# Performance work log

Measured on AMD Instinct MI355X. Metric: run time of the kernel, lower is better.

The kernel has to match this reference:

```python
import jax, jax.numpy as jnp
import numpy as np

N, E = 50000, 600000
DIMS = [128, 256, 256, 256, 256, 64]  # in, h1..h4, out


def setup_inputs() -> dict:
    key = jax.random.key(0)
    ks = jax.random.split(key, 12)
    inp = {
        "x": jax.random.normal(ks[0], (N, DIMS[0]), dtype=jnp.float32),
        "edge_index": jax.random.randint(ks[1], (2, E), 0, N, dtype=jnp.int64 if jax.config.jax_enable_x64 else jnp.int32),
    }
    for i in range(5):
        fi, fo = DIMS[i], DIMS[i + 1]
        s = 1.0 / np.sqrt(fi)  # glorot-ish uniform, matching GCNConv default scale
        inp[f"W{i+1}"] = jax.random.uniform(ks[2 + 2 * i], (fi, fo), jnp.float32, -s, s)
        inp[f"b{i+1}"] = jnp.zeros((fo,), jnp.float32)
    return inp


def _gcn_norm(edge_index, n):
    # Add self-loops and compute symmetric normalization D^-1/2 (A+I) D^-1/2.
    loop = jnp.arange(n, dtype=edge_index.dtype)
    src = jnp.concatenate([edge_index[0], loop])  # [E+N]
    dst = jnp.concatenate([edge_index[1], loop])
    deg = jax.ops.segment_sum(jnp.ones_like(dst, dtype=jnp.float32), dst, num_segments=n)
    dinv = jnp.where(deg > 0, jax.lax.rsqrt(deg), 0.0)
    norm = dinv[src] * dinv[dst]  # [E+N]
    return src, dst, norm


def _gcn_layer(x, src, dst, norm, W, b, n):
    h = x @ W                       # [N, Fo] linear transform first (fewer msg bytes)
    msg = h[src] * norm[:, None]    # gather + edge-weight scale
    out = jax.ops.segment_sum(msg, dst, num_segments=n)  # scatter-add aggregate
    return out + b


def reference(x, edge_index, W1, b1, W2, b2, W3, b3, W4, b4, W5, b5):
    n = x.shape[0]
    src, dst, norm = _gcn_norm(edge_index, n)
    params = [(W1, b1), (W2, b2), (W3, b3), (W4, b4), (W5, b5)]
    h = x
    for i, (W, b) in enumerate(params):
        h = _gcn_layer(h, src, dst, norm, W, b, n)
        if i < 4:
            h = jax.nn.relu(h)  # dropout is identity in eval mode
    return h
```

## Files before the change

### kernel.cpp

```cpp
#include <hip/hip_runtime.h>
#include <stdint.h>


typedef _Float16 v8h __attribute__((ext_vector_type(8)));
typedef _Float16 v4h __attribute__((ext_vector_type(4)));
typedef _Float16 v2h __attribute__((ext_vector_type(2)));
typedef float v4f __attribute__((ext_vector_type(4)));
typedef float v16f __attribute__((ext_vector_type(16)));

__global__ void count_edges(const int* __restrict__ dst, int E, int* __restrict__ counts) {
    int i = blockIdx.x * blockDim.x + threadIdx.x;
    if (i < E) atomicAdd(&counts[dst[i]], 1);
}

__global__ void block_sums(const int* __restrict__ counts, int n, int* __restrict__ partial) {
    __shared__ int red[256];
    int t = threadIdx.x;
    int i = blockIdx.x * 256 + t;
    red[t] = (i < n) ? counts[i] : 0;
    __syncthreads();
    #pragma unroll
    for (int off = 128; off > 0; off >>= 1) {
        if (t < off) red[t] += red[t + off];
        __syncthreads();
    }
    if (t == 0) partial[blockIdx.x] = red[0];
}

__global__ void scan_partials(int* __restrict__ partial, int nb, int* __restrict__ row_ptr, int n) {
    __shared__ int s[256];
    int t = threadIdx.x;
    int v = (t < nb) ? partial[t] : 0;
    s[t] = v;
    __syncthreads();
    #pragma unroll
    for (int off = 1; off < 256; off <<= 1) {
        int u = (t >= off) ? s[t - off] : 0;
        __syncthreads();
        s[t] += u;
        __syncthreads();
    }
    if (t < nb) partial[t] = s[t] - v;
    if (t == 0) row_ptr[n] = s[255];
}

__global__ void scan_final(const int* __restrict__ counts, int n, const int* __restrict__ partial,
                           int* __restrict__ row_ptr, float* __restrict__ dinv,
                           int* __restrict__ fill) {
    __shared__ int s[256];
    int t = threadIdx.x;
    int i = blockIdx.x * 256 + t;
    int c = (i < n) ? counts[i] : 0;
    s[t] = c;
    __syncthreads();
    #pragma unroll
    for (int off = 1; off < 256; off <<= 1) {
        int u = (t >= off) ? s[t - off] : 0;
        __syncthreads();
        s[t] += u;
        __syncthreads();
    }
    if (i < n) {
        row_ptr[i] = partial[blockIdx.x] + s[t] - c;
        dinv[i] = rsqrtf((float)(c + 1));
        fill[i] = 0;
    }
}

__global__ void build_csr(const int* __restrict__ src, const int* __restrict__ dst, int E,
                          const int* __restrict__ row_ptr, int* __restrict__ fill,
                          int2* __restrict__ esw, const float* __restrict__ dinv) {
    int i = blockIdx.x * blockDim.x + threadIdx.x;
    if (i < E) {
        int d = dst[i];
        int s = src[i];
        int pos = row_ptr[d] + atomicAdd(&fill[d], 1);
        esw[pos] = make_int2(s, __float_as_int(dinv[s]));
    }
}

struct SplitArgs {
    const float* W[5];
    _Float16* Wh[5];
    _Float16* Wl[5];
    int lgFI[5];
    int FO[5];
    int off[6];
};

__global__ void split_all(SplitArgs a) {
    int i = blockIdx.x * 256 + threadIdx.x;
    #pragma unroll
    for (int l = 0; l < 5; ++l) {
        if (i >= a.off[l] && i < a.off[l + 1]) {
            int j = i - a.off[l];
            int FI = 1 << a.lgFI[l];
            int c = j >> a.lgFI[l];
            int k = j & (FI - 1);
            float v = a.W[l][(size_t)k * a.FO[l] + c];
            _Float16 h = (_Float16)v;
            a.Wh[l][j] = h;
            a.Wl[l][j] = (_Float16)(v - (float)h);
        }
    }
}

__global__ __launch_bounds__(256) void agg_packed(
    const _Float16* __restrict__ inP, const int* __restrict__ row_ptr,
    const int2* __restrict__ esw, const float* __restrict__ dinv,
    _Float16* __restrict__ outH, _Float16* __restrict__ outL, int n) {
    int wid = (blockIdx.x * blockDim.x + threadIdx.x) >> 6;
    if (wid >= n) return;
    const int lane = threadIdx.x & 63;
    int e = __builtin_amdgcn_readfirstlane(row_ptr[wid]);
    const int end = __builtin_amdgcn_readfirstlane(row_ptr[wid + 1]);
    const float dd = dinv[wid];
    const _Float16* rb = inP + (size_t)lane * 8;
    float a0, a1, a2, a3;
    {
        v8h p = *(const v8h*)(rb + (size_t)wid * 512);
        a0 = dd * ((float)p[0] + (float)p[1]);
        a1 = dd * ((float)p[2] + (float)p[3]);
        a2 = dd * ((float)p[4] + (float)p[5]);
        a3 = dd * ((float)p[6] + (float)p[7]);
    }
#define GTH(q) (*(const v8h*)(rb + (size_t)(q).x * 512))
#define ACC(b, w)                                  \
    a0 += (w) * ((float)(b)[0] + (float)(b)[1]);   \
    a1 += (w) * ((float)(b)[2] + (float)(b)[3]);   \
    a2 += (w) * ((float)(b)[4] + (float)(b)[5]);   \
    a3 += (w) * ((float)(b)[6] + (float)(b)[7]);
    for (; e + 8 <= end; e += 8) {
        int2 q0 = esw[e + 0], q1 = esw[e + 1], q2 = esw[e + 2], q3 = esw[e + 3];
        int2 q4 = esw[e + 4], q5 = esw[e + 5], q6 = esw[e + 6], q7 = esw[e + 7];
        v8h b0 = GTH(q0), b1 = GTH(q1), b2 = GTH(q2), b3 = GTH(q3);
        v8h b4 = GTH(q4), b5 = GTH(q5), b6 = GTH(q6), b7 = GTH(q7);
        ACC(b0, __int_as_float(q0.y)) ACC(b1, __int_as_float(q1.y))
        ACC(b2, __int_as_float(q2.y)) ACC(b3, __int_as_float(q3.y))
        ACC(b4, __int_as_float(q4.y)) ACC(b5, __int_as_float(q5.y))
        ACC(b6, __int_as_float(q6.y)) ACC(b7, __int_as_float(q7.y))
    }
    if (e + 4 <= end) {
        int2 q0 = esw[e + 0], q1 = esw[e + 1], q2 = esw[e + 2], q3 = esw[e + 3];
        v8h b0 = GTH(q0), b1 = GTH(q1), b2 = GTH(q2), b3 = GTH(q3);
        ACC(b0, __int_as_float(q0.y)) ACC(b1, __int_as_float(q1.y))
        ACC(b2, __int_as_float(q2.y)) ACC(b3, __int_as_float(q3.y))
        e += 4;
    }
    if (e < end) {
        const int em = end - 1;
        int e1 = (e + 1 < end) ? e + 1 : em;
        int e2 = (e + 2 < end) ? e + 2 : em;
        int2 q0 = esw[e], q1 = esw[e1], q2 = esw[e2], q3 = esw[em];
        float w0 = __int_as_float(q0.y);
        float w1 = (e + 1 < end) ? __int_as_float(q1.y) : 0.f;
        float w2 = (e + 2 < end) ? __int_as_float(q2.y) : 0.f;
        float w3 = (e + 3 < end) ? __int_as_float(q3.y) : 0.f;
        v8h b0 = GTH(q0), b1 = GTH(q1), b2 = GTH(q2), b3 = GTH(q3);
        ACC(b0, w0) ACC(b1, w1) ACC(b2, w2) ACC(b3, w3)
    }
#undef GTH
#undef ACC
    size_t o = (size_t)wid * 256 + lane * 4;
    float s0 = dd * a0, s1 = dd * a1, s2 = dd * a2, s3 = dd * a3;
    _Float16 h0 = (_Float16)s0, h1 = (_Float16)s1, h2 = (_Float16)s2, h3 = (_Float16)s3;
    *(v4h*)&outH[o] = (v4h){h0, h1, h2, h3};
    *(v4h*)&outL[o] = (v4h){(_Float16)(s0 - (float)h0), (_Float16)(s1 - (float)h1),
                            (_Float16)(s2 - (float)h2), (_Float16)(s3 - (float)h3)};
}

__global__ __launch_bounds__(256) void agg_f32_128(
    const float* __restrict__ in, const int* __restrict__ row_ptr,
    const int2* __restrict__ esw, const float* __restrict__ dinv,
    _Float16* __restrict__ outH, _Float16* __restrict__ outL, int n) {
    int wid = (blockIdx.x * blockDim.x + threadIdx.x) >> 6;
    if (wid >= n) return;
    const int lane = threadIdx.x & 63;
    int e = __builtin_amdgcn_readfirstlane(row_ptr[wid]);
    const int end = __builtin_amdgcn_readfirstlane(row_ptr[wid + 1]);
    const float dd = dinv[wid];
    const float* rb = in + (size_t)lane * 2;
    float a0, a1;
    {
        float2 p = *(const float2*)(rb + (size_t)wid * 128);
        a0 = dd * p.x;
        a1 = dd * p.y;
    }
#define GTH(q) (*(const float2*)(rb + (size_t)(q).x * 128))
#define ACC(b, w) a0 += (w) * (b).x; a1 += (w) * (b).y;
    for (; e + 8 <= end; e += 8) {
        int2 q0 = esw[e + 0], q1 = esw[e + 1], q2 = esw[e + 2], q3 = esw[e + 3];
        int2 q4 = esw[e + 4], q5 = esw[e + 5], q6 = esw[e + 6], q7 = esw[e + 7];
        float2 b0 = GTH(q0), b1 = GTH(q1), b2 = GTH(q2), b3 = GTH(q3);
        float2 b4 = GTH(q4), b5 = GTH(q5), b6 = GTH(q6), b7 = GTH(q7);
        ACC(b0, __int_as_float(q0.y)) ACC(b1, __int_as_float(q1.y))
        ACC(b2, __int_as_float(q2.y)) ACC(b3, __int_as_float(q3.y))
        ACC(b4, __int_as_float(q4.y)) ACC(b5, __int_as_float(q5.y))
        ACC(b6, __int_as_float(q6.y)) ACC(b7, __int_as_float(q7.y))
    }
    if (e + 4 <= end) {
        int2 q0 = esw[e + 0], q1 = esw[e + 1], q2 = esw[e + 2], q3 = esw[e + 3];
        float2 b0 = GTH(q0), b1 = GTH(q1), b2 = GTH(q2), b3 = GTH(q3);
        ACC(b0, __int_as_float(q0.y)) ACC(b1, __int_as_float(q1.y))
        ACC(b2, __int_as_float(q2.y)) ACC(b3, __int_as_float(q3.y))
        e += 4;
    }
    if (e < end) {
        const int em = end - 1;
        int e1 = (e + 1 < end) ? e + 1 : em;
        int e2 = (e + 2 < end) ? e + 2 : em;
        int2 q0 = esw[e], q1 = esw[e1], q2 = esw[e2], q3 = esw[em];
        float w0 = __int_as_float(q0.y);
        float w1 = (e + 1 < end) ? __int_as_float(q1.y) : 0.f;
        float w2 = (e + 2 < end) ? __int_as_float(q2.y) : 0.f;
        float w3 = (e + 3 < end) ? __int_as_float(q3.y) : 0.f;
        float2 b0 = GTH(q0), b1 = GTH(q1), b2 = GTH(q2), b3 = GTH(q3);
        ACC(b0, w0) ACC(b1, w1) ACC(b2, w2) ACC(b3, w3)
    }
#undef GTH
#undef ACC
    size_t o = (size_t)wid * 128 + lane * 2;
    float s0 = dd * a0, s1 = dd * a1;
    _Float16 h0 = (_Float16)s0, h1 = (_Float16)s1;
    *(v2h*)&outH[o] = (v2h){h0, h1};
    *(v2h*)&outL[o] = (v2h){(_Float16)(s0 - (float)h0), (_Float16)(s1 - (float)h1)};
}

__global__ __launch_bounds__(256) void agg_f32_64(
    const float* __restrict__ in, const int* __restrict__ row_ptr,
    const int2* __restrict__ esw, const float* __restrict__ dinv,
    const float* __restrict__ bias, float* __restrict__ outF, int n) {
    int wid = (blockIdx.x * blockDim.x + threadIdx.x) >> 6;
    if (wid >= n) return;
    const int lane = threadIdx.x & 63;
    int e = __builtin_amdgcn_readfirstlane(row_ptr[wid]);
    const int end = __builtin_amdgcn_readfirstlane(row_ptr[wid + 1]);
    const float dd = dinv[wid];
    const float* rb = in + lane;
    float a0 = dd * rb[(size_t)wid * 64];
#define GTH(q) (rb[(size_t)(q).x * 64])
    for (; e + 8 <= end; e += 8) {
        int2 q0 = esw[e + 0], q1 = esw[e + 1], q2 = esw[e + 2], q3 = esw[e + 3];
        int2 q4 = esw[e + 4], q5 = esw[e + 5], q6 = esw[e + 6], q7 = esw[e + 7];
        float b0 = GTH(q0), b1 = GTH(q1), b2 = GTH(q2), b3 = GTH(q3);
        float b4 = GTH(q4), b5 = GTH(q5), b6 = GTH(q6), b7 = GTH(q7);
        a0 += __int_as_float(q0.y) * b0 + __int_as_float(q1.y) * b1;
        a0 += __int_as_float(q2.y) * b2 + __int_as_float(q3.y) * b3;
        a0 += __int_as_float(q4.y) * b4 + __int_as_float(q5.y) * b5;
        a0 += __int_as_float(q6.y) * b6 + __int_as_float(q7.y) * b7;
    }
    if (e + 4 <= end) {
        int2 q0 = esw[e + 0], q1 = esw[e + 1], q2 = esw[e + 2], q3 = esw[e + 3];
        float b0 = GTH(q0), b1 = GTH(q1), b2 = GTH(q2), b3 = GTH(q3);
        a0 += __int_as_float(q0.y) * b0 + __int_as_float(q1.y) * b1;
        a0 += __int_as_float(q2.y) * b2 + __int_as_float(q3.y) * b3;
        e += 4;
    }
    if (e < end) {
        const int em = end - 1;
        int e1 = (e + 1 < end) ? e + 1 : em;
        int e2 = (e + 2 < end) ? e + 2 : em;
        int2 q0 = esw[e], q1 = esw[e1], q2 = esw[e2], q3 = esw[em];
        float w0 = __int_as_float(q0.y);
        float w1 = (e + 1 < end) ? __int_as_float(q1.y) : 0.f;
        float w2 = (e + 2 < end) ? __int_as_float(q2.y) : 0.f;
        float w3 = (e + 3 < end) ? __int_as_float(q3.y) : 0.f;
        float b0 = GTH(q0), b1 = GTH(q1), b2 = GTH(q2), b3 = GTH(q3);
        a0 += w0 * b0 + w1 * b1 + w2 * b2 + w3 * b3;
    }
#undef GTH
    outF[(size_t)wid * 64 + lane] = dd * a0 + bias[lane];
}

__device__ __forceinline__ void gl_lds16(const _Float16* g, _Float16* l) {
    __builtin_amdgcn_global_load_lds(
        (const __attribute__((address_space(1))) uint32_t*)g,
        (__attribute__((address_space(3))) uint32_t*)l, 16, 0, 0);
}

template <int FI, int OUTMODE>
__global__ __launch_bounds__(256) void gemm_wide(
    const _Float16* __restrict__ Ah, const _Float16* __restrict__ Al,
    const _Float16* __restrict__ Wth, const _Float16* __restrict__ Wtl,
    const float* __restrict__ bias,
    uint32_t* __restrict__ Opk, _Float16* __restrict__ Oh, _Float16* __restrict__ Ol,
    int n) {
    constexpr int BK = 32;
    constexpr int NSTEP = FI / BK;
    __shared__ _Float16 lds[20480];
    const int m0 = blockIdx.x * 64;
    const int t = threadIdx.x;
    const int w = t >> 6;
    const int lane = t & 63;

    const int arow = w * 16 + (lane & 15);
    const int akc = (lane >> 4) * 8;
    const _Float16* sAh = Ah + (size_t)(m0 + arow) * FI + akc;
    const _Float16* sAl = Al + (size_t)(m0 + arow) * FI + akc;
    _Float16* dAh = &lds[w * 512];
    _Float16* dAl = &lds[2048 + w * 512];
    size_t boff[4];
    #pragma unroll
    for (int q = 0; q < 4; ++q)
        boff[q] = (size_t)((w * 4 + q) * 16 + (lane & 15)) * FI + akc;

    v16f acc[2][2];
    #pragma unroll
    for (int i = 0; i < 2; ++i)
        #pragma unroll
        for (int j = 0; j < 2; ++j) acc[i][j] = (v16f)(0.f);

    const int rsel = (lane >> 4) & 1;
    const int kq = lane >> 5;
    const int l8 = (lane & 15) * 8;

    for (int s = 0; s < NSTEP; ++s) {
        const int ko = s * BK;
        gl_lds16(sAh + ko, dAh);
        gl_lds16(sAl + ko, dAl);
        #pragma unroll
        for (int q = 0; q < 4; ++q) {
            gl_lds16(Wth + boff[q] + ko, &lds[4096 + (w * 4 + q) * 512]);
            gl_lds16(Wtl + boff[q] + ko, &lds[12288 + (w * 4 + q) * 512]);
        }
        __syncthreads();
        v8h ah[2][2], al[2][2], bh[2][2], bl[2][2];
        #pragma unroll
        for (int i = 0; i < 2; ++i)
            #pragma unroll
            for (int ks = 0; ks < 2; ++ks) {
                const int aoff = (i * 2 + rsel) * 512 + (ks * 2 + kq) * 128 + l8;
                ah[i][ks] = *(const v8h*)&lds[aoff];
                al[i][ks] = *(const v8h*)&lds[2048 + aoff];
            }
        #pragma unroll
        for (int j = 0; j < 2; ++j)
            #pragma unroll
            for (int ks = 0; ks < 2; ++ks) {
                const int bo = 4096 + (w * 4 + j * 2 + rsel) * 512 + (ks * 2 + kq) * 128 + l8;
                bh[j][ks] = *(const v8h*)&lds[bo];
                bl[j][ks] = *(const v8h*)&lds[bo + 8192];
            }
        #pragma unroll
        for (int i = 0; i < 2; ++i)
            #pragma unroll
            for (int j = 0; j < 2; ++j)
                #pragma unroll
                for (int ks = 0; ks < 2; ++ks) {
                    acc[i][j] = __builtin_amdgcn_mfma_f32_32x32x16_f16(ah[i][ks], bh[j][ks], acc[i][j], 0, 0, 0);
                    acc[i][j] = __builtin_amdgcn_mfma_f32_32x32x16_f16(ah[i][ks], bl[j][ks], acc[i][j], 0, 0, 0);
                    acc[i][j] = __builtin_amdgcn_mfma_f32_32x32x16_f16(al[i][ks], bh[j][ks], acc[i][j], 0, 0, 0);
                }
        __syncthreads();
    }

    const int col = lane & 31;
    const int rb4 = (lane >> 5) * 4;
    #pragma unroll
    for (int j = 0; j < 2; ++j) {
        const int gcol = w * 64 + j * 32 + col;
        const float bv = bias[gcol];
        #pragma unroll
        for (int i = 0; i < 2; ++i) {
            #pragma unroll
            for (int reg = 0; reg < 16; ++reg) {
                const int row = (reg & 3) + 8 * (reg >> 2) + rb4;
                const int grow = m0 + i * 32 + row;
                if (grow < n) {
                    float v = fmaxf(acc[i][j][reg] + bv, 0.f);
                    _Float16 h = (_Float16)v;
                    _Float16 l = (_Float16)(v - (float)h);
                    if (OUTMODE == 0) {
                        uint32_t u = (uint32_t)__builtin_bit_cast(uint16_t, h) |
                                     ((uint32_t)__builtin_bit_cast(uint16_t, l) << 16);
                        Opk[(size_t)grow * 256 + gcol] = u;
                    } else {
                        Oh[(size_t)grow * 256 + gcol] = h;
                        Ol[(size_t)grow * 256 + gcol] = l;
                    }
                }
            }
        }
    }
}

__global__ __launch_bounds__(256) void gemm_narrow(
    const _Float16* __restrict__ Ah, const _Float16* __restrict__ Al,
    const _Float16* __restrict__ Wth, const _Float16* __restrict__ Wtl,
    float* __restrict__ Of, int n) {
    constexpr int FI = 256, FO = 64;
    __shared__ _Float16 lds[12288];
    const int m0 = blockIdx.x * 128;
    const int t = threadIdx.x;
    const int w = t >> 6;
    const int lane = t & 63;

    const int G0 = w * 128 + lane;
    const int G1 = G0 + 64;
    const int arow0 = (G0 >> 6) * 16 + (G0 & 15), akc0 = ((G0 >> 4) & 3) * 8;
    const int arow1 = (G1 >> 6) * 16 + (G1 & 15), akc1 = ((G1 >> 4) & 3) * 8;
    const _Float16* sAh0 = Ah + (size_t)(m0 + arow0) * FI + akc0;
    const _Float16* sAh1 = Ah + (size_t)(m0 + arow1) * FI + akc1;
    const _Float16* sAl0 = Al + (size_t)(m0 + arow0) * FI + akc0;
    const _Float16* sAl1 = Al + (size_t)(m0 + arow1) * FI + akc1;
    const int bcol = w * 16 + (lane & 15), bkc = (lane >> 4) * 8;
    const _Float16* sBh = Wth + (size_t)bcol * FI + bkc;
    const _Float16* sBl = Wtl + (size_t)bcol * FI + bkc;

    _Float16* dAh0 = &lds[w * 1024];
    _Float16* dAh1 = &lds[w * 1024 + 512];
    _Float16* dAl0 = &lds[4096 + w * 1024];
    _Float16* dAl1 = &lds[4096 + w * 1024 + 512];
    _Float16* dBh = &lds[8192 + w * 512];
    _Float16* dBl = &lds[10240 + w * 512];

    const int wm = w >> 1, wn = w & 1;
    v4f acc[4][2];
    #pragma unroll
    for (int i = 0; i < 4; ++i)
        #pragma unroll
        for (int j = 0; j < 2; ++j) acc[i][j] = (v4f){0.f, 0.f, 0.f, 0.f};

    for (int s = 0; s < 8; ++s) {
        const int ko = s * 32;
        gl_lds16(sAh0 + ko, dAh0);
        gl_lds16(sAh1 + ko, dAh1);
        gl_lds16(sAl0 + ko, dAl0);
        gl_lds16(sAl1 + ko, dAl1);
        gl_lds16(sBh + ko, dBh);
        gl_lds16(sBl + ko, dBl);
        __syncthreads();
        v8h ah[4], al[4], bh[2], bl[2];
        #pragma unroll
        for (int i = 0; i < 4; ++i) {
            ah[i] = *(const v8h*)&lds[(wm * 4 + i) * 512 + lane * 8];
            al[i] = *(const v8h*)&lds[4096 + (wm * 4 + i) * 512 + lane * 8];
        }
        #pragma unroll
        for (int j = 0; j < 2; ++j) {
            bh[j] = *(const v8h*)&lds[8192 + (wn * 2 + j) * 512 + lane * 8];
            bl[j] = *(const v8h*)&lds[10240 + (wn * 2 + j) * 512 + lane * 8];
        }
        #pragma unroll
        for (int i = 0; i < 4; ++i)
            #pragma unroll
            for (int j = 0; j < 2; ++j) {
                acc[i][j] = __builtin_amdgcn_mfma_f32_16x16x32_f16(ah[i], bh[j], acc[i][j], 0, 0, 0);
                acc[i][j] = __builtin_amdgcn_mfma_f32_16x16x32_f16(ah[i], bl[j], acc[i][j], 0, 0, 0);
                acc[i][j] = __builtin_amdgcn_mfma_f32_16x16x32_f16(al[i], bh[j], acc[i][j], 0, 0, 0);
            }
        __syncthreads();
    }

    const int rl = (lane >> 4) * 4;
    const int cl = lane & 15;
    #pragma unroll
    for (int j = 0; j < 2; ++j) {
        const int gcol = wn * 32 + j * 16 + cl;
        #pragma unroll
        for (int i = 0; i < 4; ++i) {
            const int grow = m0 + wm * 64 + i * 16 + rl;
            #pragma unroll
            for (int r = 0; r < 4; ++r)
                if (grow + r < n) Of[(size_t)(grow + r) * FO + gcol] = acc[i][j][r];
        }
    }
}

extern "C" void kernel_launch(void* const* d_in, const int* in_sizes, int n_in,
                              void* d_out, int out_size, void* d_ws, size_t ws_size,
                              hipStream_t stream) {
    const float* x = (const float*)d_in[0];
    const int* ei = (const int*)d_in[1];
    const int E = in_sizes[1] / 2;
    const int n = in_sizes[0] / 128;
    const int* esrc = ei;
    const int* edst = ei + E;
    const float* b[5] = {(const float*)d_in[3], (const float*)d_in[5], (const float*)d_in[7],
                         (const float*)d_in[9], (const float*)d_in[11]};
    float* out = (float*)d_out;
    const int NPAD = ((n + 127) / 128) * 128;

    char* ws = (char*)d_ws;
    auto carve = [&](size_t bytes) {
        char* p = ws;
        ws += (bytes + 255) & ~(size_t)255;
        return p;
    };
    int* counts = (int*)carve((size_t)n * 4);
    int* row_ptr = (int*)carve((size_t)(n + 1) * 4);
    int* fill = (int*)carve((size_t)n * 4);
    float* dinv = (float*)carve((size_t)n * 4);
    int* partial = (int*)carve(1024);
    int2* esw = (int2*)carve((size_t)E * 8);
    const int FIs[5] = {128, 256, 256, 256, 256};
    const int FOs[5] = {256, 256, 256, 256, 64};
    _Float16 *Wh[5], *Wl[5];
    for (int l = 0; l < 5; ++l) {
        Wh[l] = (_Float16*)carve((size_t)FIs[l] * FOs[l] * 2);
        Wl[l] = (_Float16*)carve((size_t)FIs[l] * FOs[l] * 2);
    }
    _Float16* Ah = (_Float16*)carve((size_t)NPAD * 256 * 2);
    _Float16* Al = (_Float16*)carve((size_t)NPAD * 256 * 2);
    uint32_t* Ppk = (uint32_t*)carve((size_t)NPAD * 256 * 4);
    _Float16* Bh2 = (_Float16*)Ppk;
    _Float16* Bl2 = (_Float16*)Ppk + (size_t)NPAD * 256;
    float* scratch = (float*)Ah;

    hipMemsetAsync(counts, 0, (size_t)n * 4, stream);
    count_edges<<<(E + 255) / 256, 256, 0, stream>>>(edst, E, counts);
    const int nsb = (n + 255) / 256;
    block_sums<<<nsb, 256, 0, stream>>>(counts, n, partial);
    scan_partials<<<1, 256, 0, stream>>>(partial, nsb, row_ptr, n);
    scan_final<<<nsb, 256, 0, stream>>>(counts, n, partial, row_ptr, dinv, fill);
    build_csr<<<(E + 255) / 256, 256, 0, stream>>>(esrc, edst, E, row_ptr, fill, esw, dinv);

    SplitArgs sa;
    int off = 0;
    for (int l = 0; l < 5; ++l) {
        sa.W[l] = (const float*)d_in[2 + 2 * l];
        sa.Wh[l] = Wh[l];
        sa.Wl[l] = Wl[l];
        sa.lgFI[l] = (FIs[l] == 128) ? 7 : 8;
        sa.FO[l] = FOs[l];
        sa.off[l] = off;
        off += FIs[l] * FOs[l];
    }
    sa.off[5] = off;
    split_all<<<(off + 255) / 256, 256, 0, stream>>>(sa);

    const int aggBlocks = (n + 3) / 4;
    const int gw = NPAD / 64;
    const int gn = NPAD / 128;

    agg_f32_128<<<aggBlocks, 256, 0, stream>>>(x, row_ptr, esw, dinv, Ah, Al, n);
    gemm_wide<128, 0><<<gw, 256, 0, stream>>>(Ah, Al, Wh[0], Wl[0], b[0], Ppk, nullptr, nullptr, n);
    for (int l = 1; l <= 2; ++l) {
        agg_packed<<<aggBlocks, 256, 0, stream>>>((const _Float16*)Ppk, row_ptr, esw, dinv, Ah, Al, n);
        gemm_wide<256, 0><<<gw, 256, 0, stream>>>(Ah, Al, Wh[l], Wl[l], b[l], Ppk, nullptr, nullptr, n);
    }
    agg_packed<<<aggBlocks, 256, 0, stream>>>((const _Float16*)Ppk, row_ptr, esw, dinv, Ah, Al, n);
    gemm_wide<256, 1><<<gw, 256, 0, stream>>>(Ah, Al, Wh[3], Wl[3], b[3], nullptr, Bh2, Bl2, n);
    gemm_narrow<<<gn, 256, 0, stream>>>(Bh2, Bl2, Wh[4], Wl[4], scratch, n);
    agg_f32_64<<<(n + 3) / 4, 256, 0, stream>>>(scratch, row_ptr, esw, dinv, b[4], out, n);
}
```

Baseline: 669.0 us.

## Slice aggregation by feature columns with 8 edges per wavefront in parallel

Replaces the one-wavefront-per-row aggregation kernels with feature-sliced kernels. Each block handles a 16-column slice for 32 rows, and each wavefront processes 8 edges at once (8 lanes per edge), then reduces across lane groups with shuffles. The intent is a smaller per-slice working set that stays in cache across nearby blocks, plus better latency hiding from parallel edge gathers. In exchange it adds shuffle reductions, reads the row pointers and edge list repeatedly (once per slice), and issues smaller 8-byte gathers.

```diff
diff --git a/kernel.cpp b/kernel.cpp
--- a/kernel.cpp
+++ b/kernel.cpp
@@ -105,171 +105,117 @@
     }
 }
 
-__global__ __launch_bounds__(256) void agg_packed(
-    const _Float16* __restrict__ inP, const int* __restrict__ row_ptr,
+__device__ __forceinline__ float pk2f(uint32_t u) {
+    _Float16 h = __builtin_bit_cast(_Float16, (uint16_t)(u & 0xffffu));
+    _Float16 l = __builtin_bit_cast(_Float16, (uint16_t)(u >> 16));
+    return (float)h + (float)l;
+}
+
+__global__ __launch_bounds__(256) void agg_sliced_packed(
+    const uint32_t* __restrict__ inP, const int* __restrict__ row_ptr,
     const int2* __restrict__ esw, const float* __restrict__ dinv,
     _Float16* __restrict__ outH, _Float16* __restrict__ outL, int n) {
-    int wid = (blockIdx.x * blockDim.x + threadIdx.x) >> 6;
-    if (wid >= n) return;
-    const int lane = threadIdx.x & 63;
-    int e = __builtin_amdgcn_readfirstlane(row_ptr[wid]);
-    const int end = __builtin_amdgcn_readfirstlane(row_ptr[wid + 1]);
-    const float dd = dinv[wid];
-    const _Float16* rb = inP + (size_t)lane * 8;
-    float a0, a1, a2, a3;
-    {
-        v8h p = *(const v8h*)(rb + (size_t)wid * 512);
-        a0 = dd * ((float)p[0] + (float)p[1]);
-        a1 = dd * ((float)p[2] + (float)p[3]);
-        a2 = dd * ((float)p[4] + (float)p[5]);
-        a3 = dd * ((float)p[6] + (float)p[7]);
-    }
-#define GTH(q) (*(const v8h*)(rb + (size_t)(q).x * 512))
-#define ACC(b, w)                                  \
-    a0 += (w) * ((float)(b)[0] + (float)(b)[1]);   \
-    a1 += (w) * ((float)(b)[2] + (float)(b)[3]);   \
-    a2 += (w) * ((float)(b)[4] + (float)(b)[5]);   \
-    a3 += (w) * ((float)(b)[6] + (float)(b)[7]);
-    for (; e + 8 <= end; e += 8) {
-        int2 q0 = esw[e + 0], q1 = esw[e + 1], q2 = esw[e + 2], q3 = esw[e + 3];
-        int2 q4 = esw[e + 4], q5 = esw[e + 5], q6 = esw[e + 6], q7 = esw[e + 7];
-        v8h b0 = GTH(q0), b1 = GTH(q1), b2 = GTH(q2), b3 = GTH(q3);
-        v8h b4 = GTH(q4), b5 = GTH(q5), b6 = GTH(q6), b7 = GTH(q7);
-        ACC(b0, __int_as_float(q0.y)) ACC(b1, __int_as_float(q1.y))
-        ACC(b2, __int_as_float(q2.y)) ACC(b3, __int_as_float(q3.y))
-        ACC(b4, __int_as_float(q4.y)) ACC(b5, __int_as_float(q5.y))
-        ACC(b6, __int_as_float(q6.y)) ACC(b7, __int_as_float(q7.y))
-    }
-    if (e + 4 <= end) {
-        int2 q0 = esw[e + 0], q1 = esw[e + 1], q2 = esw[e + 2], q3 = esw[e + 3];
-        v8h b0 = GTH(q0), b1 = GTH(q1), b2 = GTH(q2), b3 = GTH(q3);
-        ACC(b0, __int_as_float(q0.y)) ACC(b1, __int_as_float(q1.y))
-        ACC(b2, __int_as_float(q2.y)) ACC(b3, __int_as_float(q3.y))
-        e += 4;
-    }
-    if (e < end) {
-        const int em = end - 1;
-        int e1 = (e + 1 < end) ? e + 1 : em;
-        int e2 = (e + 2 < end) ? e + 2 : em;
-        int2 q0 = esw[e], q1 = esw[e1], q2 = esw[e2], q3 = esw[em];
-        float w0 = __int_as_float(q0.y);
-        float w1 = (e + 1 < end) ? __int_as_float(q1.y) : 0.f;
-        float w2 = (e + 2 < end) ? __int_as_float(q2.y) : 0.f;
-        float w3 = (e + 3 < end) ? __int_as_float(q3.y) : 0.f;
-        v8h b0 = GTH(q0), b1 = GTH(q1), b2 = GTH(q2), b3 = GTH(q3);
-        ACC(b0, w0) ACC(b1, w1) ACC(b2, w2) ACC(b3, w3)
-    }
-#undef GTH
-#undef ACC
-    size_t o = (size_t)wid * 256 + lane * 4;
-    float s0 = dd * a0, s1 = dd * a1, s2 = dd * a2, s3 = dd * a3;
-    _Float16 h0 = (_Float16)s0, h1 = (_Float16)s1, h2 = (_Float16)s2, h3 = (_Float16)s3;
-    *(v4h*)&outH[o] = (v4h){h0, h1, h2, h3};
-    *(v4h*)&outL[o] = (v4h){(_Float16)(s0 - (float)h0), (_Float16)(s1 - (float)h1),
-                            (_Float16)(s2 - (float)h2), (_Float16)(s3 - (float)h3)};
-}
-
-__global__ __launch_bounds__(256) void agg_f32_128(
+    const int bid = blockIdx.x;
+    const int slice = bid & 15;
+    const int rc = bid >> 4;
+    const int w = threadIdx.x >> 6, lane = threadIdx.x & 63;
+    const int g = lane >> 3, li = lane & 7;
+    const uint32_t* sb = inP + slice * 16 + li * 2;
+    const int row0 = rc * 32 + w * 8;
+    for (int rr = 0; rr < 8; ++rr) {
+        const int row = row0 + rr;
+        if (row >= n) return;
+        const float dd = dinv[row];
+        const int e0 = __builtin_amdgcn_readfirstlane(row_ptr[row]);
+        const int end = __builtin_amdgcn_readfirstlane(row_ptr[row + 1]);
+        float a0, a1;
+        {
+            uint2 v = *(const uint2*)(sb + (size_t)row * 256);
+            const float ws = (g == 0) ? dd : 0.f;
+            a0 = ws * pk2f(v.x);
+            a1 = ws * pk2f(v.y);
+        }
+        for (int e = e0; e < end; e += 8) {
+            const int ei = e + g;
+            const int eic = (ei < end) ? ei : end - 1;
+            const int2 q = esw[eic];
+            const float wv = (ei < end) ? __int_as_float(q.y) : 0.f;
+            const uint2 v = *(const uint2*)(sb + (size_t)q.x * 256);
+            a0 += wv * pk2f(v.x);
+            a1 += wv * pk2f(v.y);
+        }
+        #pragma unroll
+        for (int off = 8; off < 64; off <<= 1) {
+            a0 += __shfl_xor(a0, off);
+            a1 += __shfl_xor(a1, off);
+        }
+        if (g == 0) {
+            const float s0 = dd * a0, s1 = dd * a1;
+            const _Float16 h0 = (_Float16)s0, h1 = (_Float16)s1;
+            const size_t o = (size_t)row * 256 + slice * 16 + li * 2;
+            *(v2h*)&outH[o] = (v2h){h0, h1};
+            *(v2h*)&outL[o] = (v2h){(_Float16)(s0 - (float)h0), (_Float16)(s1 - (float)h1)};
+        }
+    }
+}
+
+template <int F, int NSLICE, bool SPLIT_OUT>
+__global__ __launch_bounds__(256) void agg_sliced_f32(
     const float* __restrict__ in, const int* __restrict__ row_ptr,
     const int2* __restrict__ esw, const float* __restrict__ dinv,
-    _Float16* __restrict__ outH, _Float16* __restrict__ outL, int n) {
-    int wid = (blockIdx.x * blockDim.x + threadIdx.x) >> 6;
-    if (wid >= n) return;
-    const int lane = threadIdx.x & 63;
-    int e = __builtin_amdgcn_readfirstlane(row_ptr[wid]);
-    const int end = __builtin_amdgcn_readfirstlane(row_ptr[wid + 1]);
-    const float dd = dinv[wid];
-    const float* rb = in + (size_t)lane * 2;
-    float a0, a1;
-    {
-        float2 p = *(const float2*)(rb + (size_t)wid * 128);
-        a0 = dd * p.x;
-        a1 = dd * p.y;
-    }
-#define GTH(q) (*(const float2*)(rb + (size_t)(q).x * 128))
-#define ACC(b, w) a0 += (w) * (b).x; a1 += (w) * (b).y;
-    for (; e + 8 <= end; e += 8) {
-        int2 q0 = esw[e + 0], q1 = esw[e + 1], q2 = esw[e + 2], q3 = esw[e + 3];
-        int2 q4 = esw[e + 4], q5 = esw[e + 5], q6 = esw[e + 6], q7 = esw[e + 7];
-        float2 b0 = GTH(q0), b1 = GTH(q1), b2 = GTH(q2), b3 = GTH(q3);
-        float2 b4 = GTH(q4), b5 = GTH(q5), b6 = GTH(q6), b7 = GTH(q7);
-        ACC(b0, __int_as_float(q0.y)) ACC(b1, __int_as_float(q1.y))
-        ACC(b2, __int_as_float(q2.y)) ACC(b3, __int_as_float(q3.y))
-        ACC(b4, __int_as_float(q4.y)) ACC(b5, __int_as_float(q5.y))
-        ACC(b6, __int_as_float(q6.y)) ACC(b7, __int_as_float(q7.y))
-    }
-    if (e + 4 <= end) {
-        int2 q0 = esw[e + 0], q1 = esw[e + 1], q2 = esw[e + 2], q3 = esw[e + 3];
-        float2 b0 = GTH(q0), b1 = GTH(q1), b2 = GTH(q2), b3 = GTH(q3);
-        ACC(b0, __int_as_float(q0.y)) ACC(b1, __int_as_float(q1.y))
-        ACC(b2, __int_as_float(q2.y)) ACC(b3, __int_as_float(q3.y))
-        e += 4;
-    }
-    if (e < end) {
-        const int em = end - 1;
-        int e1 = (e + 1 < end) ? e + 1 : em;
-        int e2 = (e + 2 < end) ? e + 2 : em;
-        int2 q0 = esw[e], q1 = esw[e1], q2 = esw[e2], q3 = esw[em];
-        float w0 = __int_as_float(q0.y);
-        float w1 = (e + 1 < end) ? __int_as_float(q1.y) : 0.f;
-        float w2 = (e + 2 < end) ? __int_as_float(q2.y) : 0.f;
-        float w3 = (e + 3 < end) ? __int_as_float(q3.y) : 0.f;
-        float2 b0 = GTH(q0), b1 = GTH(q1), b2 = GTH(q2), b3 = GTH(q3);
-        ACC(b0, w0) ACC(b1, w1) ACC(b2, w2) ACC(b3, w3)
-    }
-#undef GTH
-#undef ACC
-    size_t o = (size_t)wid * 128 + lane * 2;
-    float s0 = dd * a0, s1 = dd * a1;
-    _Float16 h0 = (_Float16)s0, h1 = (_Float16)s1;
-    *(v2h*)&outH[o] = (v2h){h0, h1};
-    *(v2h*)&outL[o] = (v2h){(_Float16)(s0 - (float)h0), (_Float16)(s1 - (float)h1)};
-}
-
-__global__ __launch_bounds__(256) void agg_f32_64(
-    const float* __restrict__ in, const int* __restrict__ row_ptr,
-    const int2* __restrict__ esw, const float* __restrict__ dinv,
-    const float* __restrict__ bias, float* __restrict__ outF, int n) {
-    int wid = (blockIdx.x * blockDim.x + threadIdx.x) >> 6;
-    if (wid >= n) return;
-    const int lane = threadIdx.x & 63;
-    int e = __builtin_amdgcn_readfirstlane(row_ptr[wid]);
-    const int end = __builtin_amdgcn_readfirstlane(row_ptr[wid + 1]);
-    const float dd = dinv[wid];
-    const float* rb = in + lane;
-    float a0 = dd * rb[(size_t)wid * 64];
-#define GTH(q) (rb[(size_t)(q).x * 64])
-    for (; e + 8 <= end; e += 8) {
-        int2 q0 = esw[e + 0], q1 = esw[e + 1], q2 = esw[e + 2], q3 = esw[e + 3];
-        int2 q4 = esw[e + 4], q5 = esw[e + 5], q6 = esw[e + 6], q7 = esw[e + 7];
-        float b0 = GTH(q0), b1 = GTH(q1), b2 = GTH(q2), b3 = GTH(q3);
-        float b4 = GTH(q4), b5 = GTH(q5), b6 = GTH(q6), b7 = GTH(q7);
-        a0 += __int_as_float(q0.y) * b0 + __int_as_float(q1.y) * b1;
-        a0 += __int_as_float(q2.y) * b2 + __int_as_float(q3.y) * b3;
-        a0 += __int_as_float(q4.y) * b4 + __int_as_float(q5.y) * b5;
-        a0 += __int_as_float(q6.y) * b6 + __int_as_float(q7.y) * b7;
-    }
-    if (e + 4 <= end) {
-        int2 q0 = esw[e + 0], q1 = esw[e + 1], q2 = esw[e + 2], q3 = esw[e + 3];
-        float b0 = GTH(q0), b1 = GTH(q1), b2 = GTH(q2), b3 = GTH(q3);
-        a0 += __int_as_float(q0.y) * b0 + __int_as_float(q1.y) * b1;
-        a0 += __int_as_float(q2.y) * b2 + __int_as_float(q3.y) * b3;
-        e += 4;
-    }
-    if (e < end) {
-        const int em = end - 1;
-        int e1 = (e + 1 < end) ? e + 1 : em;
-        int e2 = (e + 2 < end) ? e + 2 : em;
-        int2 q0 = esw[e], q1 = esw[e1], q2 = esw[e2], q3 = esw[em];
-        float w0 = __int_as_float(q0.y);
-        float w1 = (e + 1 < end) ? __int_as_float(q1.y) : 0.f;
-        float w2 = (e + 2 < end) ? __int_as_float(q2.y) : 0.f;
-        float w3 = (e + 3 < end) ? __int_as_float(q3.y) : 0.f;
-        float b0 = GTH(q0), b1 = GTH(q1), b2 = GTH(q2), b3 = GTH(q3);
-        a0 += w0 * b0 + w1 * b1 + w2 * b2 + w3 * b3;
-    }
-#undef GTH
-    outF[(size_t)wid * 64 + lane] = dd * a0 + bias[lane];
+    const float* __restrict__ bias,
+    _Float16* __restrict__ outH, _Float16* __restrict__ outL,
+    float* __restrict__ outF, int n) {
+    const int bid = blockIdx.x;
+    const int slice = bid & (NSLICE - 1);
+    const int rc = bid / NSLICE;
+    const int w = threadIdx.x >> 6, lane = threadIdx.x & 63;
+    const int g = lane >> 3, li = lane & 7;
+    const float* sb = in + slice * 16 + li * 2;
+    const int row0 = rc * 32 + w * 8;
+    for (int rr = 0; rr < 8; ++rr) {
+        const int row = row0 + rr;
+        if (row >= n) return;
+        const float dd = dinv[row];
+        const int e0 = __builtin_amdgcn_readfirstlane(row_ptr[row]);
+        const int end = __builtin_amdgcn_readfirstlane(row_ptr[row + 1]);
+        float a0, a1;
+        {
+            const float2 v = *(const float2*)(sb + (size_t)row * F);
+            const float ws = (g == 0) ? dd : 0.f;
+            a0 = ws * v.x;
+            a1 = ws * v.y;
+        }
+        for (int e = e0; e < end; e += 8) {
+            const int ei = e + g;
+            const int eic = (ei < end) ? ei : end - 1;
+            const int2 q = esw[eic];
+            const float wv = (ei < end) ? __int_as_float(q.y) : 0.f;
+            const float2 v = *(const float2*)(sb + (size_t)q.x * F);
+            a0 += wv * v.x;
+            a1 += wv * v.y;
+        }
+        #pragma unroll
+        for (int off = 8; off < 64; off <<= 1) {
+            a0 += __shfl_xor(a0, off);
+            a1 += __shfl_xor(a1, off);
+        }
+        if (g == 0) {
+            const int c0 = slice * 16 + li * 2;
+            if constexpr (SPLIT_OUT) {
+                const float s0 = dd * a0, s1 = dd * a1;
+                const _Float16 h0 = (_Float16)s0, h1 = (_Float16)s1;
+                const size_t o = (size_t)row * F + c0;
+                *(v2h*)&outH[o] = (v2h){h0, h1};
+                *(v2h*)&outL[o] = (v2h){(_Float16)(s0 - (float)h0), (_Float16)(s1 - (float)h1)};
+            } else {
+                float2 r;
+                r.x = dd * a0 + bias[c0];
+                r.y = dd * a1 + bias[c0 + 1];
+                *(float2*)&outF[(size_t)row * F + c0] = r;
+            }
+        }
+    }
 }
 
 __device__ __forceinline__ void gl_lds16(const _Float16* g, _Float16* l) {
@@ -529,18 +475,20 @@
     sa.off[5] = off;
     split_all<<<(off + 255) / 256, 256, 0, stream>>>(sa);
 
-    const int aggBlocks = (n + 3) / 4;
+    const int rcCnt = (n + 31) / 32;
     const int gw = NPAD / 64;
     const int gn = NPAD / 128;
 
-    agg_f32_128<<<aggBlocks, 256, 0, stream>>>(x, row_ptr, esw, dinv, Ah, Al, n);
+    agg_sliced_f32<128, 8, true><<<rcCnt * 8, 256, 0, stream>>>(
+        x, row_ptr, esw, dinv, nullptr, Ah, Al, nullptr, n);
     gemm_wide<128, 0><<<gw, 256, 0, stream>>>(Ah, Al, Wh[0], Wl[0], b[0], Ppk, nullptr, nullptr, n);
     for (int l = 1; l <= 2; ++l) {
-        agg_packed<<<aggBlocks, 256, 0, stream>>>((const _Float16*)Ppk, row_ptr, esw, dinv, Ah, Al, n);
+        agg_sliced_packed<<<rcCnt * 16, 256, 0, stream>>>(Ppk, row_ptr, esw, dinv, Ah, Al, n);
         gemm_wide<256, 0><<<gw, 256, 0, stream>>>(Ah, Al, Wh[l], Wl[l], b[l], Ppk, nullptr, nullptr, n);
     }
-    agg_packed<<<aggBlocks, 256, 0, stream>>>((const _Float16*)Ppk, row_ptr, esw, dinv, Ah, Al, n);
+    agg_sliced_packed<<<rcCnt * 16, 256, 0, stream>>>(Ppk, row_ptr, esw, dinv, Ah, Al, n);
     gemm_wide<256, 1><<<gw, 256, 0, stream>>>(Ah, Al, Wh[3], Wl[3], b[3], nullptr, Bh2, Bl2, n);
     gemm_narrow<<<gn, 256, 0, stream>>>(Bh2, Bl2, Wh[4], Wl[4], scratch, n);
-    agg_f32_64<<<(n + 3) / 4, 256, 0, stream>>>(scratch, row_ptr, esw, dinv, b[4], out, n);
-}
+    agg_sliced_f32<64, 4, false><<<rcCnt * 4, 256, 0, stream>>>(
+        scratch, row_ptr, esw, dinv, b[4], nullptr, nullptr, out, n);
+}
```

Result: slower. 1.227 ms (+83.5%).

## Double-buffer LDS tiles in wide and narrow GEMM kernels

Applied to the files above, without the earlier changes.

Both GEMM kernels now use two LDS buffers. The next K-step's global-to-LDS loads are issued right after the barrier, before the current buffer is read, so load latency can overlap the MFMA work. This also removes one barrier per K iteration. In exchange, LDS per block doubles (80 KB for gemm_wide), which can lower the number of resident blocks per CU.

```diff
diff --git a/kernel.cpp b/kernel.cpp
--- a/kernel.cpp
+++ b/kernel.cpp
@@ -287,7 +287,8 @@
     int n) {
     constexpr int BK = 32;
     constexpr int NSTEP = FI / BK;
-    __shared__ _Float16 lds[20480];
+    constexpr int BUF = 20480;
+    __shared__ _Float16 lds[2 * BUF];
     const int m0 = blockIdx.x * 64;
     const int t = threadIdx.x;
     const int w = t >> 6;
@@ -297,12 +298,21 @@
     const int akc = (lane >> 4) * 8;
     const _Float16* sAh = Ah + (size_t)(m0 + arow) * FI + akc;
     const _Float16* sAl = Al + (size_t)(m0 + arow) * FI + akc;
-    _Float16* dAh = &lds[w * 512];
-    _Float16* dAl = &lds[2048 + w * 512];
     size_t boff[4];
     #pragma unroll
     for (int q = 0; q < 4; ++q)
         boff[q] = (size_t)((w * 4 + q) * 16 + (lane & 15)) * FI + akc;
+
+    auto STAGE = [&](int buf, int ko) {
+        _Float16* base = &lds[buf * BUF];
+        gl_lds16(sAh + ko, base + w * 512);
+        gl_lds16(sAl + ko, base + 2048 + w * 512);
+        #pragma unroll
+        for (int q = 0; q < 4; ++q) {
+            gl_lds16(Wth + boff[q] + ko, base + 4096 + (w * 4 + q) * 512);
+            gl_lds16(Wtl + boff[q] + ko, base + 12288 + (w * 4 + q) * 512);
+        }
+    };
 
     v16f acc[2][2];
     #pragma unroll
@@ -314,22 +324,18 @@
     const int kq = lane >> 5;
     const int l8 = (lane & 15) * 8;
 
+    STAGE(0, 0);
+    int cur = 0;
     for (int s = 0; s < NSTEP; ++s) {
-        const int ko = s * BK;
-        gl_lds16(sAh + ko, dAh);
-        gl_lds16(sAl + ko, dAl);
-        #pragma unroll
-        for (int q = 0; q < 4; ++q) {
-            gl_lds16(Wth + boff[q] + ko, &lds[4096 + (w * 4 + q) * 512]);
-            gl_lds16(Wtl + boff[q] + ko, &lds[12288 + (w * 4 + q) * 512]);
-        }
-        __syncthreads();
+        __syncthreads();
+        if (s + 1 < NSTEP) STAGE(cur ^ 1, (s + 1) * BK);
+        const int cb = cur * BUF;
         v8h ah[2][2], al[2][2], bh[2][2], bl[2][2];
         #pragma unroll
         for (int i = 0; i < 2; ++i)
             #pragma unroll
             for (int ks = 0; ks < 2; ++ks) {
-                const int aoff = (i * 2 + rsel) * 512 + (ks * 2 + kq) * 128 + l8;
+                const int aoff = cb + (i * 2 + rsel) * 512 + (ks * 2 + kq) * 128 + l8;
                 ah[i][ks] = *(const v8h*)&lds[aoff];
                 al[i][ks] = *(const v8h*)&lds[2048 + aoff];
             }
@@ -337,7 +343,7 @@
         for (int j = 0; j < 2; ++j)
             #pragma unroll
             for (int ks = 0; ks < 2; ++ks) {
-                const int bo = 4096 + (w * 4 + j * 2 + rsel) * 512 + (ks * 2 + kq) * 128 + l8;
+                const int bo = cb + 4096 + (w * 4 + j * 2 + rsel) * 512 + (ks * 2 + kq) * 128 + l8;
                 bh[j][ks] = *(const v8h*)&lds[bo];
                 bl[j][ks] = *(const v8h*)&lds[bo + 8192];
             }
@@ -351,7 +357,7 @@
                     acc[i][j] = __builtin_amdgcn_mfma_f32_32x32x16_f16(ah[i][ks], bl[j][ks], acc[i][j], 0, 0, 0);
                     acc[i][j] = __builtin_amdgcn_mfma_f32_32x32x16_f16(al[i][ks], bh[j][ks], acc[i][j], 0, 0, 0);
                 }
-        __syncthreads();
+        cur ^= 1;
     }
 
     const int col = lane & 31;
@@ -389,7 +395,8 @@
     const _Float16* __restrict__ Wth, const _Float16* __restrict__ Wtl,
     float* __restrict__ Of, int n) {
     constexpr int FI = 256, FO = 64;
-    __shared__ _Float16 lds[12288];
+    constexpr int BUF = 12288;
+    __shared__ _Float16 lds[2 * BUF];
     const int m0 = blockIdx.x * 128;
     const int t = threadIdx.x;
     const int w = t >> 6;
@@ -407,12 +414,15 @@
     const _Float16* sBh = Wth + (size_t)bcol * FI + bkc;
     const _Float16* sBl = Wtl + (size_t)bcol * FI + bkc;
 
-    _Float16* dAh0 = &lds[w * 1024];
-    _Float16* dAh1 = &lds[w * 1024 + 512];
-    _Float16* dAl0 = &lds[4096 + w * 1024];
-    _Float16* dAl1 = &lds[4096 + w * 1024 + 512];
-    _Float16* dBh = &lds[8192 + w * 512];
-    _Float16* dBl = &lds[10240 + w * 512];
+    auto STAGE = [&](int buf, int ko) {
+        _Float16* base = &lds[buf * BUF];
+        gl_lds16(sAh0 + ko, base + w * 1024);
+        gl_lds16(sAh1 + ko, base + w * 1024 + 512);
+        gl_lds16(sAl0 + ko, base + 4096 + w * 1024);
+        gl_lds16(sAl1 + ko, base + 4096 + w * 1024 + 512);
+        gl_lds16(sBh + ko, base + 8192 + w * 512);
+        gl_lds16(sBl + ko, base + 10240 + w * 512);
+    };
 
     const int wm = w >> 1, wn = w & 1;
     v4f acc[4][2];
@@ -421,25 +431,22 @@
         #pragma unroll
         for (int j = 0; j < 2; ++j) acc[i][j] = (v4f){0.f, 0.f, 0.f, 0.f};
 
+    STAGE(0, 0);
+    int cur = 0;
     for (int s = 0; s < 8; ++s) {
-        const int ko = s * 32;
-        gl_lds16(sAh0 + ko, dAh0);
-        gl_lds16(sAh1 + ko, dAh1);
-        gl_lds16(sAl0 + ko, dAl0);
-        gl_lds16(sAl1 + ko, dAl1);
-        gl_lds16(sBh + ko, dBh);
-        gl_lds16(sBl + ko, dBl);
-        __syncthreads();
+        __syncthreads();
+        if (s + 1 < 8) STAGE(cur ^ 1, (s + 1) * 32);
+        const int cb = cur * BUF;
         v8h ah[4], al[4], bh[2], bl[2];
         #pragma unroll
         for (int i = 0; i < 4; ++i) {
-            ah[i] = *(const v8h*)&lds[(wm * 4 + i) * 512 + lane * 8];
-            al[i] = *(const v8h*)&lds[4096 + (wm * 4 + i) * 512 + lane * 8];
+            ah[i] = *(const v8h*)&lds[cb + (wm * 4 + i) * 512 + lane * 8];
+            al[i] = *(const v8h*)&lds[cb + 4096 + (wm * 4 + i) * 512 + lane * 8];
         }
         #pragma unroll
         for (int j = 0; j < 2; ++j) {
-            bh[j] = *(const v8h*)&lds[8192 + (wn * 2 + j) * 512 + lane * 8];
-            bl[j] = *(const v8h*)&lds[10240 + (wn * 2 + j) * 512 + lane * 8];
+            bh[j] = *(const v8h*)&lds[cb + 8192 + (wn * 2 + j) * 512 + lane * 8];
+            bl[j] = *(const v8h*)&lds[cb + 10240 + (wn * 2 + j) * 512 + lane * 8];
         }
         #pragma unroll
         for (int i = 0; i < 4; ++i)
@@ -449,7 +456,7 @@
                 acc[i][j] = __builtin_amdgcn_mfma_f32_16x16x32_f16(ah[i], bl[j], acc[i][j], 0, 0, 0);
                 acc[i][j] = __builtin_amdgcn_mfma_f32_16x16x32_f16(al[i], bh[j], acc[i][j], 0, 0, 0);
             }
-        __syncthreads();
+        cur ^= 1;
     }
 
     const int rl = (lane >> 4) * 4;
```

New measurement: 669.2 us. Within noise of the previous version (+0.0%).
